# Optimization experiments

Hardware: AMD Instinct MI355X
Metric: run time of the kernel (lower is better)

## Reference

```python
import jax, jax.numpy as jnp
import numpy as np
import math

D_MODEL = 1024
D_K = 256
B, T = 4, 4096

def setup_inputs() -> dict:
    key = jax.random.key(0)
    ks = jax.random.split(key, 7)
    s = 1.0 / math.sqrt(D_MODEL)
    return {
        "inputs": jax.random.normal(ks[0], (B, T, D_MODEL), dtype=jnp.float32),
        "Wq": jax.random.uniform(ks[1], (D_MODEL, D_K), jnp.float32, -s, s),
        "bq": jax.random.uniform(ks[2], (D_K,), jnp.float32, -s, s),
        "Wk": jax.random.uniform(ks[3], (D_MODEL, D_K), jnp.float32, -s, s),
        "bk": jax.random.uniform(ks[4], (D_K,), jnp.float32, -s, s),
        "Wv": jax.random.uniform(ks[5], (D_MODEL, D_K), jnp.float32, -s, s),
        "bv": jax.random.uniform(ks[6], (D_K,), jnp.float32, -s, s),
    }

def reference(inputs, Wq, bq, Wk, bk, Wv, bv):
    q = inputs @ Wq + bq                      # [B,T,d_k]
    k = inputs @ Wk + bk
    v = inputs @ Wv + bv
    scores = jnp.einsum('btd,bsd->bts', q, k)  # [B,T,T]
    Tdim = inputs.shape[1]
    causal = jnp.tril(jnp.ones((Tdim, Tdim), dtype=bool))
    # faithful to original: mask with -1e9 BEFORE dividing by sqrt(d_k)
    scores = jnp.where(causal[None], scores, jnp.float32(-1e9))
    attn = jax.nn.softmax(scores / math.sqrt(D_K), axis=-1)
    return jnp.einsum('bts,bsd->btd', attn, v)
```

## Files before the change

kernel.cpp:

```cpp
#include <hip/hip_runtime.h>
#include <stdint.h>

typedef uint16_t u16;
typedef uint32_t u32;
typedef float    f32x4  __attribute__((ext_vector_type(4)));
typedef short    bf16x8 __attribute__((ext_vector_type(8)));
typedef u32      u32x4  __attribute__((ext_vector_type(4)));
typedef u32      u32x2  __attribute__((ext_vector_type(2)));
typedef u16      u16x8  __attribute__((ext_vector_type(8)));
typedef u16      u16x4  __attribute__((ext_vector_type(4)));

#define MFMA16(a, b, c) __builtin_amdgcn_mfma_f32_16x16x32_bf16((a), (b), (c), 0, 0, 0)


__device__ __forceinline__ u16 f2bf(float f) {
  u32 x = __float_as_uint(f);
  return (u16)((x + 0x7FFFu + ((x >> 16) & 1u)) >> 16);
}

__global__ __launch_bounds__(256) void cvt_w_kernel(const float* __restrict__ Wq,
                                                    const float* __restrict__ Wk,
                                                    const float* __restrict__ Wv,
                                                    u16* __restrict__ Wt) {
  int idx = blockIdx.x * 256 + threadIdx.x;
  int m = idx >> 18;
  int n = (idx >> 10) & 255;
  int k = idx & 1023;
  const float* W = (m == 0) ? Wq : (m == 1) ? Wk : Wv;
  Wt[idx] = f2bf(W[k * 256 + n]);
}

__global__ __launch_bounds__(256) void qkv_gemm_kernel(
    const float* __restrict__ X, const u16* __restrict__ Wt,
    const float* __restrict__ bq, const float* __restrict__ bk, const float* __restrict__ bv,
    u16* __restrict__ Qb, u16* __restrict__ Kb, u16* __restrict__ Vtb) {
  __shared__ __align__(16) char sm[32768];
  const int tid = threadIdx.x;
  const int wid = tid >> 6, lane = tid & 63, g = lane >> 4, lr = lane & 15;
  const int wr = wid >> 1, wc = wid & 1;
  const int m0 = blockIdx.x * 128, n0 = blockIdx.y * 128, z = blockIdx.z;
  const u16* W = Wt + z * 262144;

  f32x4 acc[4][4];
#pragma unroll
  for (int mi = 0; mi < 4; ++mi)
#pragma unroll
    for (int ni = 0; ni < 4; ++ni) {
      acc[mi][ni][0] = 0.f; acc[mi][ni][1] = 0.f; acc[mi][ni][2] = 0.f; acc[mi][ni][3] = 0.f;
    }

  for (int k0 = 0; k0 < 1024; k0 += 64) {
    __syncthreads();
#pragma unroll
    for (int r = 0; r < 4; ++r) {
      int ch = r * 256 + tid;
      int row = ch >> 3, c = ch & 7;
      const float* xp = X + (size_t)(m0 + row) * 1024 + k0 + c * 8;
      f32x4 xa = *(const f32x4*)xp;
      f32x4 xb = *(const f32x4*)(xp + 4);
      u16x8 xc;
      xc[0] = f2bf(xa[0]); xc[1] = f2bf(xa[1]); xc[2] = f2bf(xa[2]); xc[3] = f2bf(xa[3]);
      xc[4] = f2bf(xb[0]); xc[5] = f2bf(xb[1]); xc[6] = f2bf(xb[2]); xc[7] = f2bf(xb[3]);
      *(u16x8*)(sm + row * 128 + 16 * (c ^ (row & 7))) = xc;
      u32x4 vw = *(const u32x4*)(W + (size_t)(n0 + row) * 1024 + k0 + c * 8);
      *(u32x4*)(sm + 16384 + row * 128 + 16 * (c ^ (row & 7))) = vw;
    }
    __syncthreads();
#pragma unroll
    for (int kk = 0; kk < 2; ++kk) {
      bf16x8 af[4], bfr[4];
#pragma unroll
      for (int mi = 0; mi < 4; ++mi) {
        int row = wr * 64 + mi * 16 + lr;
        af[mi] = *(const bf16x8*)(sm + row * 128 + 16 * ((kk * 4 + g) ^ (row & 7)));
      }
#pragma unroll
      for (int ni = 0; ni < 4; ++ni) {
        int row = wc * 64 + ni * 16 + lr;
        bfr[ni] = *(const bf16x8*)(sm + 16384 + row * 128 + 16 * ((kk * 4 + g) ^ (row & 7)));
      }
#pragma unroll
      for (int mi = 0; mi < 4; ++mi)
#pragma unroll
        for (int ni = 0; ni < 4; ++ni)
          acc[mi][ni] = MFMA16(af[mi], bfr[ni], acc[mi][ni]);
    }
  }

  const float* bias = (z == 0) ? bq : (z == 1) ? bk : bv;
  if (z < 2) {
    u16* O = (z == 0) ? Qb : Kb;
    const float qscale = (z == 0) ? 0.0625f : 1.0f;
#pragma unroll
    for (int ni = 0; ni < 4; ++ni) {
      int col = n0 + wc * 64 + ni * 16 + lr;
      float bb = bias[col];
#pragma unroll
      for (int mi = 0; mi < 4; ++mi)
#pragma unroll
        for (int j = 0; j < 4; ++j) {
          int row = m0 + wr * 64 + mi * 16 + 4 * g + j;
          O[(size_t)row * 256 + col] = f2bf((acc[mi][ni][j] + bb) * qscale);
        }
    }
  } else {
    __syncthreads();
#pragma unroll
    for (int ni = 0; ni < 4; ++ni) {
      int cl = wc * 64 + ni * 16 + lr;
      float bb = bias[n0 + cl];
#pragma unroll
      for (int mi = 0; mi < 4; ++mi)
#pragma unroll
        for (int j = 0; j < 4; ++j) {
          int rl = wr * 64 + mi * 16 + 4 * g + j;
          *(u16*)(sm + cl * 256 + rl * 2) = f2bf(acc[mi][ni][j] + bb);
        }
    }
    __syncthreads();
    int bidx = m0 >> 12, tb = m0 & 4095;
#pragma unroll
    for (int r = 0; r < 8; ++r) {
      int ch = r * 256 + tid;
      int cl = ch >> 4, tp = ch & 15;
      u32x4 v = *(const u32x4*)(sm + cl * 256 + tp * 16);
      *(u32x4*)(Vtb + (size_t)bidx * 1048576 + (size_t)(n0 + cl) * 4096 + tb + tp * 8) = v;
    }
  }
}

__global__ __launch_bounds__(512) void flash_kernel(
    const u16* __restrict__ Qb, const u16* __restrict__ Kb,
    const u16* __restrict__ Vtb, u16* __restrict__ Opart, float2* __restrict__ ML,
    int s, int gx) {
  __shared__ __align__(16) char sm[73728];
  const int tid = threadIdx.x, wid = tid >> 6, lane = tid & 63, g = lane >> 4, lr = lane & 15;
  const int xcd = blockIdx.x & 7;
  const int b = xcd >> 1;
  const int i = ((blockIdx.x >> 3) << 1) + (xcd & 1);
  const int QG = 1 << (s - 1);
  const int NG = 32 >> (s - 1);
  const int ND = (QG * NG * (NG - 1)) >> 1;
  int gg, qq, sc;
  if (i < ND) {
    gg = 1;
    while (gg < NG - 1 && i >= ((QG * (gg + 1) * gg) >> 1)) ++gg;
    int local = i - ((QG * gg * (gg - 1)) >> 1);
    qq = local / gg;
    sc = local - qq * gg;
  } else {
    int j = i - ND;
    int jd = j / NG;
    qq = (QG - 1) - jd;
    gg = j - jd * NG;
    sc = gg;
  }
  const int qb = gg * QG + qq;
  const int t0 = qb * 128;
  const int w0 = t0 + wid * 16;
  const int C = 64 << s;
  const int sbase = sc * C;

  bf16x8 qf[8];
  const u16* Qrow = Qb + (size_t)(b * 4096 + w0 + lr) * 256;
#pragma unroll
  for (int kk = 0; kk < 8; ++kk) qf[kk] = *(const bf16x8*)(Qrow + kk * 32 + g * 8);

  f32x4 o[16];
#pragma unroll
  for (int n = 0; n < 16; ++n) { o[n][0] = 0.f; o[n][1] = 0.f; o[n][2] = 0.f; o[n][3] = 0.f; }
  float m_ = -1e30f, l_ = 0.f;

  const u16* Kbase = Kb + (size_t)b * 4096 * 256;
  const u16* Vbase = Vtb + (size_t)b * 1048576;

  u32x4 pk[4], pv[4];
#define LOADTILE(os_)                                                                      \
  {                                                                                        \
    _Pragma("unroll")                                                                      \
    for (int q = 0; q < 4; ++q) {                                                          \
      int half = q >> 1, rr = q & 1;                                                       \
      int ch = rr * 512 + tid;                          \
      int srow = ch >> 5, c = ch & 31;                                                     \
      pk[q] = *(const u32x4*)(Kbase + (size_t)((os_) + half * 32 + srow) * 256 + c * 8);   \
      int d = ch >> 2, c2 = ch & 3;                                                        \
      pv[q] = *(const u32x4*)(Vbase + (size_t)d * 4096 + (os_) + half * 32 + c2 * 8);      \
    }                                                                                      \
  }

  const int nto = min(C >> 6, (t0 + 128 - sbase) >> 6);
  LOADTILE(sbase);

  for (int ot = 0; ot < nto; ++ot) {
    const int os0 = sbase + ot * 64;
    __syncthreads();
#pragma unroll
    for (int q = 0; q < 4; ++q) {
      int half = q >> 1, rr = q & 1;
      int ch = rr * 512 + tid;
      int srow = ch >> 5, c = ch & 31;
      *(u32x4*)(sm + half * 16384 + srow * 512 + 16 * (c ^ (srow & 7))) = pk[q];
      int d = ch >> 2, c2 = ch & 3;
      *(u32x4*)(sm + 32768 + half * 16384 + d * 64 + 16 * (c2 ^ ((d >> 1) & 3))) = pv[q];
    }
    if (ot + 1 < nto) LOADTILE(os0 + 64);
    __syncthreads();

#pragma unroll 1
    for (int half = 0; half < 2; ++half) {
      const int s0 = os0 + 32 * half;
      if (s0 > w0 + 15) break;
      const char* kb = sm + half * 16384;
      const char* vb = sm + 32768 + half * 16384;

      f32x4 sa[2];
#pragma unroll
      for (int ni = 0; ni < 2; ++ni) { sa[ni][0] = 0.f; sa[ni][1] = 0.f; sa[ni][2] = 0.f; sa[ni][3] = 0.f; }
#pragma unroll
      for (int ni = 0; ni < 2; ++ni) {
        int srw = ni * 16 + lr;
#pragma unroll
        for (int kk = 0; kk < 8; ++kk) {
          bf16x8 kf = *(const bf16x8*)(kb + srw * 512 + 16 * ((kk * 4 + g) ^ (srw & 7)));
          sa[ni] = MFMA16(kf, qf[kk], sa[ni]);
        }
      }
      const int t = w0 + lr;
      if (s0 + 31 > w0) {
#pragma unroll
        for (int ni = 0; ni < 2; ++ni)
#pragma unroll
          for (int j = 0; j < 4; ++j) {
            int ss = s0 + ni * 16 + 4 * g + j;
            if (t < ss) sa[ni][j] = -1e30f;
          }
      }
      float mt = fmaxf(fmaxf(fmaxf(sa[0][0], sa[0][1]), fmaxf(sa[0][2], sa[0][3])),
                       fmaxf(fmaxf(sa[1][0], sa[1][1]), fmaxf(sa[1][2], sa[1][3])));
      mt = fmaxf(mt, __shfl_xor(mt, 16, 64));
      mt = fmaxf(mt, __shfl_xor(mt, 32, 64));
      if (__any(mt > m_ + 8.0f)) {
        float mn = fmaxf(m_, mt);
        float scale = __expf(m_ - mn);
        m_ = mn;
        l_ *= scale;
#pragma unroll
        for (int n = 0; n < 16; ++n)
#pragma unroll
          for (int j = 0; j < 4; ++j) o[n][j] *= scale;
      }
#pragma unroll
      for (int ni = 0; ni < 2; ++ni)
#pragma unroll
        for (int j = 0; j < 4; ++j) sa[ni][j] = __expf(sa[ni][j] - m_);
      float su = (sa[0][0] + sa[0][1]) + (sa[0][2] + sa[0][3]) +
                 (sa[1][0] + sa[1][1]) + (sa[1][2] + sa[1][3]);
      su += __shfl_xor(su, 16, 64);
      su += __shfl_xor(su, 32, 64);
      l_ += su;
#pragma unroll
      for (int ni = 0; ni < 2; ++ni) {
        int c = ni * 2 + (g >> 1);
        u32x2 pw;
        pw[0] = (u32)f2bf(sa[ni][0]) | ((u32)f2bf(sa[ni][1]) << 16);
        pw[1] = (u32)f2bf(sa[ni][2]) | ((u32)f2bf(sa[ni][3]) << 16);
        *(u32x2*)(sm + 65536 + wid * 1024 + lr * 64 + 16 * (c ^ (lr & 3)) + 8 * (g & 1)) = pw;
      }
      asm volatile("s_waitcnt lgkmcnt(0)" ::: "memory");
      bf16x8 pf = *(const bf16x8*)(sm + 65536 + wid * 1024 + lr * 64 + 16 * (g ^ (lr & 3)));
#pragma unroll
      for (int n = 0; n < 16; ++n) {
        int d = n * 16 + lr;
        bf16x8 vf = *(const bf16x8*)(vb + d * 64 + 16 * (g ^ ((d >> 1) & 3)));
        o[n] = MFMA16(vf, pf, o[n]);
      }
    }
  }
#undef LOADTILE

  u16* Orow = Opart + ((size_t)(b * gx + i) * 128 + wid * 16) * 256;
#pragma unroll
  for (int n = 0; n < 16; ++n) {
    u16x4 pkk;
    pkk[0] = f2bf(o[n][0]); pkk[1] = f2bf(o[n][1]); pkk[2] = f2bf(o[n][2]); pkk[3] = f2bf(o[n][3]);
    *(u16x4*)(Orow + lr * 256 + n * 16 + 4 * g) = pkk;
  }
  if (lane < 16) {
    float2 ml; ml.x = m_; ml.y = l_;
    ML[(size_t)(b * gx + i) * 128 + wid * 16 + lane] = ml;
  }
}

__global__ __launch_bounds__(256) void combine_kernel(const u16* __restrict__ Opart,
                                                      const float2* __restrict__ ML,
                                                      float* __restrict__ out,
                                                      int s, int gx) {
  const int wid = threadIdx.x >> 6, lane = threadIdx.x & 63;
  const int rg = blockIdx.x * 4 + wid;
  const int b = rg >> 12, t = rg & 4095;
  const int qb = t >> 7;
  const int QG = 1 << (s - 1), NG = 32 >> (s - 1);
  const int ND = (QG * NG * (NG - 1)) >> 1;
  const int gg = qb >> (s - 1), qq = qb & (QG - 1);
  const int n = gg + 1;
  const int ibase = ((QG * gg * (gg - 1)) >> 1) + qq * gg;
  const int idiag = ND + (QG - 1 - qq) * NG + gg;
  const int tl = t & 127;
  int sl[8];
  float mv[8], lv[8], w[8];
  float M = -1e30f;
#pragma unroll
  for (int sc = 0; sc < 8; ++sc)
    if (sc < n) {
      sl[sc] = b * gx + ((sc < gg) ? (ibase + sc) : idiag);
      float2 ml = ML[(size_t)sl[sc] * 128 + tl];
      mv[sc] = ml.x; lv[sc] = ml.y;
      M = fmaxf(M, ml.x);
    }
  float L = 0.f;
#pragma unroll
  for (int sc = 0; sc < 8; ++sc)
    if (sc < n) { w[sc] = __expf(mv[sc] - M); L += w[sc] * lv[sc]; }
  const float inv = 1.0f / L;
  const int c0 = lane * 4;
  float a0 = 0.f, a1 = 0.f, a2 = 0.f, a3 = 0.f;
#pragma unroll
  for (int sc = 0; sc < 8; ++sc)
    if (sc < n) {
      u16x4 v = *(const u16x4*)(Opart + ((size_t)sl[sc] * 128 + tl) * 256 + c0);
      a0 += w[sc] * __uint_as_float((u32)v[0] << 16);
      a1 += w[sc] * __uint_as_float((u32)v[1] << 16);
      a2 += w[sc] * __uint_as_float((u32)v[2] << 16);
      a3 += w[sc] * __uint_as_float((u32)v[3] << 16);
    }
  f32x4 r; r[0] = a0 * inv; r[1] = a1 * inv; r[2] = a2 * inv; r[3] = a3 * inv;
  *(f32x4*)(out + (size_t)rg * 256 + c0) = r;
}

extern "C" void kernel_launch(void* const* d_in, const int* in_sizes, int n_in,
                              void* d_out, int out_size, void* d_ws, size_t ws_size,
                              hipStream_t stream) {
  const float* X  = (const float*)d_in[0];
  const float* Wq = (const float*)d_in[1];
  const float* bq = (const float*)d_in[2];
  const float* Wk = (const float*)d_in[3];
  const float* bk = (const float*)d_in[4];
  const float* Wv = (const float*)d_in[5];
  const float* bv = (const float*)d_in[6];
  float* out = (float*)d_out;
  char* ws = (char*)d_ws;

  const size_t OFF_WT  = 33554432;
  const size_t OFF_Q   = OFF_WT + 1572864;
  const size_t OFF_K   = OFF_Q + 8388608;
  const size_t OFF_VT  = OFF_K + 8388608;
  const size_t PREFIX  = OFF_VT + 8388608;

  const size_t NEEDED_A = PREFIX + 589824 + 37748736;
  const size_t NEEDED_B = PREFIX + 327680;
  if (ws_size < NEEDED_B) return;

  u16* Wt  = (u16*)(ws + OFF_WT);
  u16* Qb  = (u16*)(ws + OFF_Q);
  u16* Kb  = (u16*)(ws + OFF_K);
  u16* Vtb = (u16*)(ws + OFF_VT);

  int s, gx;
  u16* Opart;
  float2* ML;
  if (ws_size >= NEEDED_A) {
    s = 3; gx = 144;
    ML = (float2*)(ws + PREFIX);
    Opart = (u16*)(ws + PREFIX + 589824);
  } else {
    s = 4; gx = 80;
    ML = (float2*)(ws + PREFIX);
    Opart = (u16*)ws;
  }

  cvt_w_kernel<<<3072, 256, 0, stream>>>(Wq, Wk, Wv, Wt);
  qkv_gemm_kernel<<<dim3(128, 2, 3), 256, 0, stream>>>(X, Wt, bq, bk, bv, Qb, Kb, Vtb);
  flash_kernel<<<4 * gx, 512, 0, stream>>>(Qb, Kb, Vtb, Opart, ML, s, gx);
  combine_kernel<<<4096, 256, 0, stream>>>(Opart, ML, out, s, gx);
}
```

Measured before the change: 150.0 us.

## Switch flash attention to 32x32 MFMA with 4 waves of 32 rows each

Rewrites the flash kernel to use 32x32x16 bf16 MFMA, with each of 4 waves owning 32 query rows instead of 8 waves owning 16. The P matrix is repacked through cross-lane shuffles instead of an LDS round-trip. K/V tiles are now loaded straight into LDS each iteration rather than register-prefetched for the next tile. This is meant to raise MFMA efficiency and cut LDS traffic. In exchange it loses the load/compute overlap, raises register pressure, and halves threads per block.

```diff
diff --git a/kernel.cpp b/kernel.cpp
--- a/kernel.cpp
+++ b/kernel.cpp
@@ -4,6 +4,7 @@
 typedef uint16_t u16;
 typedef uint32_t u32;
 typedef float    f32x4  __attribute__((ext_vector_type(4)));
+typedef float    f32x16 __attribute__((ext_vector_type(16)));
 typedef short    bf16x8 __attribute__((ext_vector_type(8)));
 typedef u32      u32x4  __attribute__((ext_vector_type(4)));
 typedef u32      u32x2  __attribute__((ext_vector_type(2)));
@@ -11,6 +12,7 @@
 typedef u16      u16x4  __attribute__((ext_vector_type(4)));
 
 #define MFMA16(a, b, c) __builtin_amdgcn_mfma_f32_16x16x32_bf16((a), (b), (c), 0, 0, 0)
+#define MFMA32(a, b, c) __builtin_amdgcn_mfma_f32_32x32x16_bf16((a), (b), (c), 0, 0, 0)
 
 
 __device__ __forceinline__ u16 f2bf(float f) {
@@ -129,12 +131,13 @@
   }
 }
 
-__global__ __launch_bounds__(512) void flash_kernel(
+__global__ __launch_bounds__(256) void flash_kernel(
     const u16* __restrict__ Qb, const u16* __restrict__ Kb,
     const u16* __restrict__ Vtb, u16* __restrict__ Opart, float2* __restrict__ ML,
     int s, int gx) {
-  __shared__ __align__(16) char sm[73728];
-  const int tid = threadIdx.x, wid = tid >> 6, lane = tid & 63, g = lane >> 4, lr = lane & 15;
+  __shared__ __align__(16) char sm[65536];
+  const int tid = threadIdx.x, wid = tid >> 6, lane = tid & 63;
+  const int ql = lane & 31, h = lane >> 5;
   const int xcd = blockIdx.x & 7;
   const int b = xcd >> 1;
   const int i = ((blockIdx.x >> 3) << 1) + (xcd & 1);
@@ -157,87 +160,72 @@
   }
   const int qb = gg * QG + qq;
   const int t0 = qb * 128;
-  const int w0 = t0 + wid * 16;
+  const int w0 = t0 + wid * 32;
   const int C = 64 << s;
   const int sbase = sc * C;
 
-  bf16x8 qf[8];
-  const u16* Qrow = Qb + (size_t)(b * 4096 + w0 + lr) * 256;
-#pragma unroll
-  for (int kk = 0; kk < 8; ++kk) qf[kk] = *(const bf16x8*)(Qrow + kk * 32 + g * 8);
-
-  f32x4 o[16];
-#pragma unroll
-  for (int n = 0; n < 16; ++n) { o[n][0] = 0.f; o[n][1] = 0.f; o[n][2] = 0.f; o[n][3] = 0.f; }
+  const u16* Qrow = Qb + (size_t)(b * 4096 + w0 + ql) * 256;
+  bf16x8 qf[16];
+#pragma unroll
+  for (int kk = 0; kk < 16; ++kk) qf[kk] = *(const bf16x8*)(Qrow + kk * 16 + h * 8);
+
+  f32x16 o[8];
+#pragma unroll
+  for (int n = 0; n < 8; ++n)
+#pragma unroll
+    for (int r = 0; r < 16; ++r) o[n][r] = 0.f;
   float m_ = -1e30f, l_ = 0.f;
 
   const u16* Kbase = Kb + (size_t)b * 4096 * 256;
   const u16* Vbase = Vtb + (size_t)b * 1048576;
 
-  u32x4 pk[4], pv[4];
-#define LOADTILE(os_)                                                                      \
-  {                                                                                        \
-    _Pragma("unroll")                                                                      \
-    for (int q = 0; q < 4; ++q) {                                                          \
-      int half = q >> 1, rr = q & 1;                                                       \
-      int ch = rr * 512 + tid;                          \
-      int srow = ch >> 5, c = ch & 31;                                                     \
-      pk[q] = *(const u32x4*)(Kbase + (size_t)((os_) + half * 32 + srow) * 256 + c * 8);   \
-      int d = ch >> 2, c2 = ch & 3;                                                        \
-      pv[q] = *(const u32x4*)(Vbase + (size_t)d * 4096 + (os_) + half * 32 + c2 * 8);      \
-    }                                                                                      \
-  }
-
   const int nto = min(C >> 6, (t0 + 128 - sbase) >> 6);
-  LOADTILE(sbase);
-
   for (int ot = 0; ot < nto; ++ot) {
     const int os0 = sbase + ot * 64;
     __syncthreads();
 #pragma unroll
-    for (int q = 0; q < 4; ++q) {
-      int half = q >> 1, rr = q & 1;
-      int ch = rr * 512 + tid;
+    for (int r = 0; r < 8; ++r) {
+      int ch = r * 256 + tid;
       int srow = ch >> 5, c = ch & 31;
-      *(u32x4*)(sm + half * 16384 + srow * 512 + 16 * (c ^ (srow & 7))) = pk[q];
-      int d = ch >> 2, c2 = ch & 3;
-      *(u32x4*)(sm + 32768 + half * 16384 + d * 64 + 16 * (c2 ^ ((d >> 1) & 3))) = pv[q];
-    }
-    if (ot + 1 < nto) LOADTILE(os0 + 64);
+      u32x4 v = *(const u32x4*)(Kbase + (size_t)(os0 + srow) * 256 + c * 8);
+      *(u32x4*)(sm + srow * 512 + 16 * (c ^ (srow & 7))) = v;
+    }
+#pragma unroll
+    for (int r = 0; r < 8; ++r) {
+      int ch = r * 256 + tid;
+      int d = ch >> 3, c2 = ch & 7;
+      u32x4 v = *(const u32x4*)(Vbase + (size_t)d * 4096 + os0 + c2 * 8);
+      *(u32x4*)(sm + 32768 + d * 128 + 16 * (c2 ^ (d & 7))) = v;
+    }
     __syncthreads();
 
 #pragma unroll 1
-    for (int half = 0; half < 2; ++half) {
-      const int s0 = os0 + 32 * half;
-      if (s0 > w0 + 15) break;
-      const char* kb = sm + half * 16384;
-      const char* vb = sm + 32768 + half * 16384;
-
-      f32x4 sa[2];
-#pragma unroll
-      for (int ni = 0; ni < 2; ++ni) { sa[ni][0] = 0.f; sa[ni][1] = 0.f; sa[ni][2] = 0.f; sa[ni][3] = 0.f; }
-#pragma unroll
-      for (int ni = 0; ni < 2; ++ni) {
-        int srw = ni * 16 + lr;
-#pragma unroll
-        for (int kk = 0; kk < 8; ++kk) {
-          bf16x8 kf = *(const bf16x8*)(kb + srw * 512 + 16 * ((kk * 4 + g) ^ (srw & 7)));
-          sa[ni] = MFMA16(kf, qf[kk], sa[ni]);
+    for (int sh = 0; sh < 2; ++sh) {
+      const int s0 = os0 + sh * 32;
+      if (s0 > w0 + 31) break;
+      const char* kb = sm + sh * 16384;
+      f32x16 sa0, sa1;
+#pragma unroll
+      for (int r = 0; r < 16; ++r) { sa0[r] = 0.f; sa1[r] = 0.f; }
+#pragma unroll
+      for (int kk = 0; kk < 16; kk += 2) {
+        bf16x8 kf0 = *(const bf16x8*)(kb + ql * 512 + 16 * ((kk * 2 + h) ^ (ql & 7)));
+        bf16x8 kf1 = *(const bf16x8*)(kb + ql * 512 + 16 * (((kk + 1) * 2 + h) ^ (ql & 7)));
+        sa0 = MFMA32(kf0, qf[kk], sa0);
+        sa1 = MFMA32(kf1, qf[kk + 1], sa1);
+      }
+      f32x16 sa = sa0 + sa1;
+      const int t = w0 + ql;
+      if (s0 + 31 > w0) {
+#pragma unroll
+        for (int r = 0; r < 16; ++r) {
+          int ss = s0 + (r & 3) + 8 * (r >> 2) + 4 * h;
+          if (t < ss) sa[r] = -1e30f;
         }
       }
-      const int t = w0 + lr;
-      if (s0 + 31 > w0) {
-#pragma unroll
-        for (int ni = 0; ni < 2; ++ni)
-#pragma unroll
-          for (int j = 0; j < 4; ++j) {
-            int ss = s0 + ni * 16 + 4 * g + j;
-            if (t < ss) sa[ni][j] = -1e30f;
-          }
-      }
-      float mt = fmaxf(fmaxf(fmaxf(sa[0][0], sa[0][1]), fmaxf(sa[0][2], sa[0][3])),
-                       fmaxf(fmaxf(sa[1][0], sa[1][1]), fmaxf(sa[1][2], sa[1][3])));
-      mt = fmaxf(mt, __shfl_xor(mt, 16, 64));
+      float mt = sa[0];
+#pragma unroll
+      for (int r = 1; r < 16; ++r) mt = fmaxf(mt, sa[r]);
       mt = fmaxf(mt, __shfl_xor(mt, 32, 64));
       if (__any(mt > m_ + 8.0f)) {
         float mn = fmaxf(m_, mt);
@@ -245,49 +233,63 @@
         m_ = mn;
         l_ *= scale;
 #pragma unroll
-        for (int n = 0; n < 16; ++n)
-#pragma unroll
-          for (int j = 0; j < 4; ++j) o[n][j] *= scale;
-      }
-#pragma unroll
-      for (int ni = 0; ni < 2; ++ni)
-#pragma unroll
-        for (int j = 0; j < 4; ++j) sa[ni][j] = __expf(sa[ni][j] - m_);
-      float su = (sa[0][0] + sa[0][1]) + (sa[0][2] + sa[0][3]) +
-                 (sa[1][0] + sa[1][1]) + (sa[1][2] + sa[1][3]);
-      su += __shfl_xor(su, 16, 64);
+        for (int n = 0; n < 8; ++n)
+#pragma unroll
+          for (int r = 0; r < 16; ++r) o[n][r] *= scale;
+      }
+#pragma unroll
+      for (int r = 0; r < 16; ++r) sa[r] = __expf(sa[r] - m_);
+      float su = 0.f;
+#pragma unroll
+      for (int r = 0; r < 16; ++r) su += sa[r];
       su += __shfl_xor(su, 32, 64);
       l_ += su;
-#pragma unroll
-      for (int ni = 0; ni < 2; ++ni) {
-        int c = ni * 2 + (g >> 1);
-        u32x2 pw;
-        pw[0] = (u32)f2bf(sa[ni][0]) | ((u32)f2bf(sa[ni][1]) << 16);
-        pw[1] = (u32)f2bf(sa[ni][2]) | ((u32)f2bf(sa[ni][3]) << 16);
-        *(u32x2*)(sm + 65536 + wid * 1024 + lr * 64 + 16 * (c ^ (lr & 3)) + 8 * (g & 1)) = pw;
-      }
-      asm volatile("s_waitcnt lgkmcnt(0)" ::: "memory");
-      bf16x8 pf = *(const bf16x8*)(sm + 65536 + wid * 1024 + lr * 64 + 16 * (g ^ (lr & 3)));
-#pragma unroll
-      for (int n = 0; n < 16; ++n) {
-        int d = n * 16 + lr;
-        bf16x8 vf = *(const bf16x8*)(vb + d * 64 + 16 * (g ^ ((d >> 1) & 3)));
-        o[n] = MFMA16(vf, pf, o[n]);
-      }
-    }
-  }
-#undef LOADTILE
-
-  u16* Orow = Opart + ((size_t)(b * gx + i) * 128 + wid * 16) * 256;
-#pragma unroll
-  for (int n = 0; n < 16; ++n) {
-    u16x4 pkk;
-    pkk[0] = f2bf(o[n][0]); pkk[1] = f2bf(o[n][1]); pkk[2] = f2bf(o[n][2]); pkk[3] = f2bf(o[n][3]);
-    *(u16x4*)(Orow + lr * 256 + n * 16 + 4 * g) = pkk;
-  }
-  if (lane < 16) {
+      u32 w0p = (u32)f2bf(sa[0])  | ((u32)f2bf(sa[1])  << 16);
+      u32 w1p = (u32)f2bf(sa[2])  | ((u32)f2bf(sa[3])  << 16);
+      u32 w2p = (u32)f2bf(sa[4])  | ((u32)f2bf(sa[5])  << 16);
+      u32 w3p = (u32)f2bf(sa[6])  | ((u32)f2bf(sa[7])  << 16);
+      u32 w4p = (u32)f2bf(sa[8])  | ((u32)f2bf(sa[9])  << 16);
+      u32 w5p = (u32)f2bf(sa[10]) | ((u32)f2bf(sa[11]) << 16);
+      u32 w6p = (u32)f2bf(sa[12]) | ((u32)f2bf(sa[13]) << 16);
+      u32 w7p = (u32)f2bf(sa[14]) | ((u32)f2bf(sa[15]) << 16);
+      const int pl = lane ^ 32;
+      u32 sA = h ? w0p : w2p;  u32 rA = __shfl(sA, pl, 64);
+      u32 sB = h ? w1p : w3p;  u32 rB = __shfl(sB, pl, 64);
+      u32 sC = h ? w4p : w6p;  u32 rC = __shfl(sC, pl, 64);
+      u32 sD = h ? w5p : w7p;  u32 rD = __shfl(sD, pl, 64);
+      union { u32 u[4]; bf16x8 v; } P0, P1;
+      if (h == 0) {
+        P0.u[0] = w0p; P0.u[1] = w1p; P0.u[2] = rA;  P0.u[3] = rB;
+        P1.u[0] = w4p; P1.u[1] = w5p; P1.u[2] = rC;  P1.u[3] = rD;
+      } else {
+        P0.u[0] = rA;  P0.u[1] = rB;  P0.u[2] = w2p; P0.u[3] = w3p;
+        P1.u[0] = rC;  P1.u[1] = rD;  P1.u[2] = w6p; P1.u[3] = w7p;
+      }
+#pragma unroll
+      for (int n = 0; n < 8; ++n) {
+        int dv = n * 32 + ql;
+        const char* vrow = sm + 32768 + dv * 128;
+        bf16x8 vf0 = *(const bf16x8*)(vrow + 16 * ((sh * 4 + h) ^ (dv & 7)));
+        bf16x8 vf1 = *(const bf16x8*)(vrow + 16 * ((sh * 4 + 2 + h) ^ (dv & 7)));
+        o[n] = MFMA32(vf0, P0.v, o[n]);
+        o[n] = MFMA32(vf1, P1.v, o[n]);
+      }
+    }
+  }
+
+  u16* Orow = Opart + ((size_t)(b * gx + i) * 128 + wid * 32) * 256;
+#pragma unroll
+  for (int n = 0; n < 8; ++n)
+#pragma unroll
+    for (int j = 0; j < 4; ++j) {
+      u16x4 pkk;
+      pkk[0] = f2bf(o[n][4 * j + 0]); pkk[1] = f2bf(o[n][4 * j + 1]);
+      pkk[2] = f2bf(o[n][4 * j + 2]); pkk[3] = f2bf(o[n][4 * j + 3]);
+      *(u16x4*)(Orow + ql * 256 + n * 32 + 8 * j + 4 * h) = pkk;
+    }
+  if (lane < 32) {
     float2 ml; ml.x = m_; ml.y = l_;
-    ML[(size_t)(b * gx + i) * 128 + wid * 16 + lane] = ml;
+    ML[(size_t)(b * gx + i) * 128 + wid * 32 + lane] = ml;
   }
 }
 
@@ -380,6 +382,6 @@
 
   cvt_w_kernel<<<3072, 256, 0, stream>>>(Wq, Wk, Wv, Wt);
   qkv_gemm_kernel<<<dim3(128, 2, 3), 256, 0, stream>>>(X, Wt, bq, bk, bv, Qb, Kb, Vtb);
-  flash_kernel<<<4 * gx, 512, 0, stream>>>(Qb, Kb, Vtb, Opart, ML, s, gx);
+  flash_kernel<<<4 * gx, 256, 0, stream>>>(Qb, Kb, Vtb, Opart, ML, s, gx);
   combine_kernel<<<4096, 256, 0, stream>>>(Opart, ML, out, s, gx);
 }
```

New measurement: 161.7 us. 1.08x slower.
